# Optimization experiments

Measured on AMD Instinct MI355X. Metric: run time of the kernel, lower is better.

## Reference

```python
import jax, jax.numpy as jnp
import numpy as np

FOCUS_RADIUS = 20.0
FOCUS_WEIGHT = 10.0
SPREAD_PENALTY = 1.0
EPS = 1e-8


def setup_inputs() -> dict:
    key = jax.random.key(0)
    k1, k2 = jax.random.split(key)
    B, WL, H, W = 16, 8, 512, 512
    predictions = jax.random.uniform(k1, (B, WL, H, W), dtype=jnp.float32)
    targets = jax.random.uniform(k2, (B, WL, H, W), dtype=jnp.float32)
    return {"predictions": predictions, "targets": targets}


def reference(predictions, targets):
    B, WL, H, W = predictions.shape
    dt = predictions.dtype
    ys = jnp.arange(H, dtype=dt)[:, None]   # [H,1]
    xs = jnp.arange(W, dtype=dt)[None, :]   # [1,W]

    # base MSE loss
    base_loss = jnp.mean((predictions - targets) ** 2)

    # target energy centroids (detached in the original via .item())
    tsum = targets.sum((-2, -1))                      # [B,WL]
    valid = tsum >= EPS                               # center exists
    ts_safe = jnp.where(valid, tsum, 1.0)
    cy = jax.lax.stop_gradient((targets * ys).sum((-2, -1)) / ts_safe)  # [B,WL]
    cx = jax.lax.stop_gradient((targets * xs).sum((-2, -1)) / ts_safe)  # [B,WL]

    # squared distance to target center, per image  [B,WL,H,W]
    dist_sq = (ys - cy[..., None, None]) ** 2 + (xs - cx[..., None, None]) ** 2
    focus_mask = (dist_sq <= FOCUS_RADIUS * FOCUS_RADIUS).astype(dt)

    pred_total = predictions.sum((-2, -1))            # [B,WL]
    focus_energy = (predictions * focus_mask).sum((-2, -1))
    spread = (predictions * dist_sq).sum((-2, -1))
    pt_safe = jnp.where(pred_total > EPS, pred_total, 1.0)

    active = valid & (pred_total > EPS)
    focus_loss = jnp.sum(jnp.where(active, (1.0 - focus_energy / pt_safe) ** 2, 0.0))
    spread_loss = jnp.sum(jnp.where(active, spread / pt_safe, 0.0))

    return base_loss + FOCUS_WEIGHT * focus_loss + SPREAD_PENALTY * spread_loss
```

## Files before the change

kernel.cpp:

```cpp
#include <hip/hip_runtime.h>


#define HH 512
#define WW 512
#define IMG_PIX (HH * WW)
#define VEC_PER_IMG (IMG_PIX / 4)
#define BLOCKS_PER_IMG 16
#define VEC_PER_BLK (VEC_PER_IMG / BLOCKS_PER_IMG)
#define THREADS 256
#define ITERS (VEC_PER_BLK / THREADS)
#define EPSF 1e-8f
#define R2 400.0f

typedef float f4 __attribute__((ext_vector_type(4)));

__device__ __forceinline__ float wave_reduce_sum(float v) {
    v += __shfl_down(v, 32);
    v += __shfl_down(v, 16);
    v += __shfl_down(v, 8);
    v += __shfl_down(v, 4);
    v += __shfl_down(v, 2);
    v += __shfl_down(v, 1);
    return v;
}

__device__ __forceinline__ double wave_reduce_sum_d(double v) {
    v += __shfl_down(v, 32);
    v += __shfl_down(v, 16);
    v += __shfl_down(v, 8);
    v += __shfl_down(v, 4);
    v += __shfl_down(v, 2);
    v += __shfl_down(v, 1);
    return v;
}

__global__ void __launch_bounds__(THREADS) stream_kernel(
        const f4* __restrict__ pred, const f4* __restrict__ tgt,
        float* __restrict__ part) {
    const int img = blockIdx.x / BLOCKS_PER_IMG;
    const int sub = blockIdx.x % BLOCKS_PER_IMG;
    const int base = img * VEC_PER_IMG + sub * VEC_PER_BLK;

    float ts = 0.f, ty = 0.f, tx = 0.f, mse = 0.f;
    float m0 = 0.f, my = 0.f, mx = 0.f, m2 = 0.f;

#pragma unroll 8
    for (int j = 0; j < ITERS; ++j) {
        const int i = j * THREADS + threadIdx.x;
        const int vidx = base + i;
        const f4 tv = __builtin_nontemporal_load(&tgt[vidx]);
        const f4 pv = pred[vidx];
        const int pix = (sub * VEC_PER_BLK + i) << 2;
        const float y  = (float)(pix >> 9);
        const float x0 = (float)(pix & 511);
        const float x1 = x0 + 1.f, x2 = x0 + 2.f, x3 = x0 + 3.f;

        const float tsum = tv[0] + tv[1] + tv[2] + tv[3];
        ts += tsum;
        ty += y * tsum;
        tx += x0 * tv[0] + x1 * tv[1] + x2 * tv[2] + x3 * tv[3];

        const float d0 = pv[0] - tv[0], d1 = pv[1] - tv[1],
                    d2 = pv[2] - tv[2], d3 = pv[3] - tv[3];
        mse += d0 * d0 + d1 * d1 + d2 * d2 + d3 * d3;

        const float psum = pv[0] + pv[1] + pv[2] + pv[3];
        m0 += psum;
        my += y * psum;
        mx += x0 * pv[0] + x1 * pv[1] + x2 * pv[2] + x3 * pv[3];
        const float y2 = y * y;
        m2 += pv[0] * (y2 + x0 * x0) + pv[1] * (y2 + x1 * x1)
            + pv[2] * (y2 + x2 * x2) + pv[3] * (y2 + x3 * x3);
    }

    float vals[8] = {ts, ty, tx, mse, m0, my, mx, m2};
    __shared__ float red[4][8];
    const int wid = threadIdx.x >> 6, lane = threadIdx.x & 63;
#pragma unroll
    for (int k = 0; k < 8; ++k) vals[k] = wave_reduce_sum(vals[k]);
    if (lane == 0)
#pragma unroll
        for (int k = 0; k < 8; ++k) red[wid][k] = vals[k];
    __syncthreads();
    if (threadIdx.x < 8) {
        const int k = threadIdx.x;
        part[blockIdx.x * 8 + k] = red[0][k] + red[1][k] + red[2][k] + red[3][k];
    }
}

__global__ void __launch_bounds__(64) focus_kernel(
        const float* __restrict__ pred, const float* __restrict__ part,
        float* __restrict__ fe_out) {
    const int img = blockIdx.x;
    const int lane = threadIdx.x;
    float ts = 0.f, ty = 0.f, tx = 0.f;
    if (lane < BLOCKS_PER_IMG) {
        const float* p = part + (img * BLOCKS_PER_IMG + lane) * 8;
        ts = p[0]; ty = p[1]; tx = p[2];
    }
    ts = __shfl(wave_reduce_sum(ts), 0);
    ty = __shfl(wave_reduce_sum(ty), 0);
    tx = __shfl(wave_reduce_sum(tx), 0);

    float fe = 0.f;
    if (ts >= EPSF) {
        const float cy = ty / ts;
        const float cx = tx / ts;
        const int ylo = max(0, (int)ceilf(cy - 20.f) - 1);
        const int yhi = min(HH - 1, (int)floorf(cy + 20.f) + 1);
        const int xlo = max(0, (int)ceilf(cx - 20.f) - 1);
        const int xhi = min(WW - 1, (int)floorf(cx + 20.f) + 1);
        const float* p = pred + (size_t)img * IMG_PIX;
        const int xx = xlo + lane;
        if (xx <= xhi) {
            const float dx = (float)xx - cx;
            const float dx2 = dx * dx;
            for (int y = ylo; y <= yhi; ++y) {
                const float dy = (float)y - cy;
                if (dy * dy + dx2 <= R2) fe += p[(y << 9) + xx];
            }
        }
    }
    fe = wave_reduce_sum(fe);
    if (lane == 0) fe_out[img] = fe;
}

__global__ void __launch_bounds__(128) final_kernel(
        const float* __restrict__ part, const float* __restrict__ fe,
        float* __restrict__ out, int nimg, float inv_n) {
    const int i = threadIdx.x;
    double v = 0.0, m = 0.0;
    if (i < nimg) {
        float ts = 0.f, mse = 0.f, m0 = 0.f, myv = 0.f, mxv = 0.f, m2 = 0.f;
        float tyv = 0.f, txv = 0.f;
        const float* p = part + i * BLOCKS_PER_IMG * 8;
#pragma unroll
        for (int s = 0; s < BLOCKS_PER_IMG; ++s) {
            ts  += p[s * 8 + 0];
            tyv += p[s * 8 + 1];
            txv += p[s * 8 + 2];
            mse += p[s * 8 + 3];
            m0  += p[s * 8 + 4];
            myv += p[s * 8 + 5];
            mxv += p[s * 8 + 6];
            m2  += p[s * 8 + 7];
        }
        m = (double)mse;
        if (ts >= EPSF && m0 > EPSF) {
            const double cy = (double)tyv / (double)ts;
            const double cx = (double)txv / (double)ts;
            const double spread = (double)m2 - 2.0 * cy * (double)myv
                                - 2.0 * cx * (double)mxv
                                + (cy * cy + cx * cx) * (double)m0;
            const double r = 1.0 - (double)fe[i] / (double)m0;
            v = 10.0 * r * r + spread / (double)m0;
        }
    }
    __shared__ double redv[2], redm[2];
    v = wave_reduce_sum_d(v);
    m = wave_reduce_sum_d(m);
    if ((i & 63) == 0) { redv[i >> 6] = v; redm[i >> 6] = m; }
    __syncthreads();
    if (i == 0)
        out[0] = (float)((redm[0] + redm[1]) * (double)inv_n + redv[0] + redv[1]);
}

extern "C" void kernel_launch(void* const* d_in, const int* in_sizes, int n_in,
                              void* d_out, int out_size, void* d_ws, size_t ws_size,
                              hipStream_t stream) {
    const float* pred = (const float*)d_in[0];
    const float* tgt  = (const float*)d_in[1];
    float* out = (float*)d_out;
    float* ws  = (float*)d_ws;

    const int n = in_sizes[0];
    const int nimg = n / IMG_PIX;
    const int nblk = nimg * BLOCKS_PER_IMG;

    float* part = ws;
    float* fe   = ws + nblk * 8;

    stream_kernel<<<nblk, THREADS, 0, stream>>>(
        (const f4*)pred, (const f4*)tgt, part);
    focus_kernel<<<nimg, 64, 0, stream>>>(pred, part, fe);
    final_kernel<<<1, 128, 0, stream>>>(part, fe, out, nimg, 1.0f / (float)n);
}
```

Baseline: 63.92 us.

## Double-buffer stream loads, simplify moment math, move per-image finalization into focus kernel

The streaming kernel now prefetches the next batch of four vector loads per thread into a register double buffer while computing on the current batch. The number of blocks per image drops from 16 to 8, and the per-pixel moment arithmetic is rewritten in factored form to cut FLOPs. The focus kernel now uses 256 threads, with the four waves splitting the rows, and it computes each image's loss term, which leaves the final kernel as a simple reduction. The risks are higher register pressure from the double buffer and fewer blocks in flight to hide memory latency.

```diff
diff --git a/kernel.cpp b/kernel.cpp
--- a/kernel.cpp
+++ b/kernel.cpp
@@ -5,10 +5,12 @@
 #define WW 512
 #define IMG_PIX (HH * WW)
 #define VEC_PER_IMG (IMG_PIX / 4)
-#define BLOCKS_PER_IMG 16
+#define BLOCKS_PER_IMG 8
 #define VEC_PER_BLK (VEC_PER_IMG / BLOCKS_PER_IMG)
 #define THREADS 256
 #define ITERS (VEC_PER_BLK / THREADS)
+#define BATCH 4
+#define NBATCH (ITERS / BATCH)
 #define EPSF 1e-8f
 #define R2 400.0f
 
@@ -39,38 +41,57 @@
         float* __restrict__ part) {
     const int img = blockIdx.x / BLOCKS_PER_IMG;
     const int sub = blockIdx.x % BLOCKS_PER_IMG;
-    const int base = img * VEC_PER_IMG + sub * VEC_PER_BLK;
+    const int base = img * VEC_PER_IMG + sub * VEC_PER_BLK + (int)threadIdx.x;
+
+    f4 tb[2][BATCH], pb[2][BATCH];
+#pragma unroll
+    for (int u = 0; u < BATCH; ++u) {
+        tb[0][u] = __builtin_nontemporal_load(&tgt[base + u * THREADS]);
+        pb[0][u] = pred[base + u * THREADS];
+    }
 
     float ts = 0.f, ty = 0.f, tx = 0.f, mse = 0.f;
     float m0 = 0.f, my = 0.f, mx = 0.f, m2 = 0.f;
 
-#pragma unroll 8
-    for (int j = 0; j < ITERS; ++j) {
-        const int i = j * THREADS + threadIdx.x;
-        const int vidx = base + i;
-        const f4 tv = __builtin_nontemporal_load(&tgt[vidx]);
-        const f4 pv = pred[vidx];
-        const int pix = (sub * VEC_PER_BLK + i) << 2;
-        const float y  = (float)(pix >> 9);
-        const float x0 = (float)(pix & 511);
-        const float x1 = x0 + 1.f, x2 = x0 + 2.f, x3 = x0 + 3.f;
-
-        const float tsum = tv[0] + tv[1] + tv[2] + tv[3];
-        ts += tsum;
-        ty += y * tsum;
-        tx += x0 * tv[0] + x1 * tv[1] + x2 * tv[2] + x3 * tv[3];
-
-        const float d0 = pv[0] - tv[0], d1 = pv[1] - tv[1],
-                    d2 = pv[2] - tv[2], d3 = pv[3] - tv[3];
-        mse += d0 * d0 + d1 * d1 + d2 * d2 + d3 * d3;
-
-        const float psum = pv[0] + pv[1] + pv[2] + pv[3];
-        m0 += psum;
-        my += y * psum;
-        mx += x0 * pv[0] + x1 * pv[1] + x2 * pv[2] + x3 * pv[3];
-        const float y2 = y * y;
-        m2 += pv[0] * (y2 + x0 * x0) + pv[1] * (y2 + x1 * x1)
-            + pv[2] * (y2 + x2 * x2) + pv[3] * (y2 + x3 * x3);
+#pragma unroll
+    for (int b = 0; b < NBATCH; ++b) {
+        const int cur = b & 1, nxt = cur ^ 1;
+        if (b + 1 < NBATCH) {
+#pragma unroll
+            for (int u = 0; u < BATCH; ++u) {
+                const int v = base + ((b + 1) * BATCH + u) * THREADS;
+                tb[nxt][u] = __builtin_nontemporal_load(&tgt[v]);
+                pb[nxt][u] = pred[v];
+            }
+        }
+#pragma unroll
+        for (int u = 0; u < BATCH; ++u) {
+            const int iv = sub * VEC_PER_BLK + (b * BATCH + u) * THREADS
+                         + (int)threadIdx.x;
+            const float y  = (float)(iv >> 7);
+            const float x0 = (float)((iv & 127) << 2);
+            const f4 tv = tb[cur][u];
+            const f4 pv = pb[cur][u];
+
+            const float tsum = tv[0] + tv[1] + tv[2] + tv[3];
+            const float tw1  = tv[1] + 2.f * tv[2] + 3.f * tv[3];
+            ts += tsum;
+            ty += y * tsum;
+            tx += x0 * tsum + tw1;
+
+            const float d0 = pv[0] - tv[0], d1 = pv[1] - tv[1],
+                        d2 = pv[2] - tv[2], d3 = pv[3] - tv[3];
+            mse += d0 * d0 + d1 * d1 + d2 * d2 + d3 * d3;
+
+            const float psum = pv[0] + pv[1] + pv[2] + pv[3];
+            const float pw1  = pv[1] + 2.f * pv[2] + 3.f * pv[3];
+            const float pw2  = pv[1] + 4.f * pv[2] + 9.f * pv[3];
+            m0 += psum;
+            my += y * psum;
+            mx += x0 * psum + pw1;
+            const float r2c = y * y + x0 * x0;
+            m2 += r2c * psum + 2.f * x0 * pw1 + pw2;
+        }
     }
 
     float vals[8] = {ts, ty, tx, mse, m0, my, mx, m2};
@@ -88,81 +109,86 @@
     }
 }
 
-__global__ void __launch_bounds__(64) focus_kernel(
+__global__ void __launch_bounds__(THREADS) focus_kernel(
         const float* __restrict__ pred, const float* __restrict__ part,
-        float* __restrict__ fe_out) {
+        double* __restrict__ vout, double* __restrict__ mout) {
     const int img = blockIdx.x;
-    const int lane = threadIdx.x;
-    float ts = 0.f, ty = 0.f, tx = 0.f;
-    if (lane < BLOCKS_PER_IMG) {
-        const float* p = part + (img * BLOCKS_PER_IMG + lane) * 8;
-        ts = p[0]; ty = p[1]; tx = p[2];
-    }
-    ts = __shfl(wave_reduce_sum(ts), 0);
-    ty = __shfl(wave_reduce_sum(ty), 0);
-    tx = __shfl(wave_reduce_sum(tx), 0);
-
+    const int tid = threadIdx.x;
+    __shared__ float mom[8];
+    {
+        float v[8] = {0.f, 0.f, 0.f, 0.f, 0.f, 0.f, 0.f, 0.f};
+        if (tid < BLOCKS_PER_IMG) {
+            const float* p = part + (img * BLOCKS_PER_IMG + tid) * 8;
+#pragma unroll
+            for (int k = 0; k < 8; ++k) v[k] = p[k];
+        }
+        if (tid < 64) {
+#pragma unroll
+            for (int k = 0; k < 8; ++k) v[k] = wave_reduce_sum(v[k]);
+            if (tid == 0)
+#pragma unroll
+                for (int k = 0; k < 8; ++k) mom[k] = v[k];
+        }
+    }
+    __syncthreads();
+
+    const float ts = mom[0];
     float fe = 0.f;
+    float cy = 0.f, cx = 0.f;
     if (ts >= EPSF) {
-        const float cy = ty / ts;
-        const float cx = tx / ts;
+        cy = mom[1] / ts;
+        cx = mom[2] / ts;
         const int ylo = max(0, (int)ceilf(cy - 20.f) - 1);
         const int yhi = min(HH - 1, (int)floorf(cy + 20.f) + 1);
         const int xlo = max(0, (int)ceilf(cx - 20.f) - 1);
         const int xhi = min(WW - 1, (int)floorf(cx + 20.f) + 1);
         const float* p = pred + (size_t)img * IMG_PIX;
+        const int lane = tid & 63, w = tid >> 6;
         const int xx = xlo + lane;
         if (xx <= xhi) {
             const float dx = (float)xx - cx;
             const float dx2 = dx * dx;
-            for (int y = ylo; y <= yhi; ++y) {
+            for (int y = ylo + w; y <= yhi; y += 4) {
                 const float dy = (float)y - cy;
                 if (dy * dy + dx2 <= R2) fe += p[(y << 9) + xx];
             }
         }
     }
+    __shared__ float redf[4];
     fe = wave_reduce_sum(fe);
-    if (lane == 0) fe_out[img] = fe;
+    if ((tid & 63) == 0) redf[tid >> 6] = fe;
+    __syncthreads();
+    if (tid == 0) {
+        const float fet = redf[0] + redf[1] + redf[2] + redf[3];
+        const float m0 = mom[4];
+        double v = 0.0;
+        if (ts >= EPSF && m0 > EPSF) {
+            const double dcy = (double)mom[1] / (double)ts;
+            const double dcx = (double)mom[2] / (double)ts;
+            const double spread = (double)mom[7] - 2.0 * dcy * (double)mom[5]
+                                - 2.0 * dcx * (double)mom[6]
+                                + (dcy * dcy + dcx * dcx) * (double)m0;
+            const double r = 1.0 - (double)fet / (double)m0;
+            v = 10.0 * r * r + spread / (double)m0;
+        }
+        vout[img] = v;
+        mout[img] = (double)mom[3];
+    }
 }
 
 __global__ void __launch_bounds__(128) final_kernel(
-        const float* __restrict__ part, const float* __restrict__ fe,
-        float* __restrict__ out, int nimg, float inv_n) {
+        const double* __restrict__ vout, const double* __restrict__ mout,
+        float* __restrict__ out, int nimg, double inv_n) {
     const int i = threadIdx.x;
     double v = 0.0, m = 0.0;
-    if (i < nimg) {
-        float ts = 0.f, mse = 0.f, m0 = 0.f, myv = 0.f, mxv = 0.f, m2 = 0.f;
-        float tyv = 0.f, txv = 0.f;
-        const float* p = part + i * BLOCKS_PER_IMG * 8;
-#pragma unroll
-        for (int s = 0; s < BLOCKS_PER_IMG; ++s) {
-            ts  += p[s * 8 + 0];
-            tyv += p[s * 8 + 1];
-            txv += p[s * 8 + 2];
-            mse += p[s * 8 + 3];
-            m0  += p[s * 8 + 4];
-            myv += p[s * 8 + 5];
-            mxv += p[s * 8 + 6];
-            m2  += p[s * 8 + 7];
-        }
-        m = (double)mse;
-        if (ts >= EPSF && m0 > EPSF) {
-            const double cy = (double)tyv / (double)ts;
-            const double cx = (double)txv / (double)ts;
-            const double spread = (double)m2 - 2.0 * cy * (double)myv
-                                - 2.0 * cx * (double)mxv
-                                + (cy * cy + cx * cx) * (double)m0;
-            const double r = 1.0 - (double)fe[i] / (double)m0;
-            v = 10.0 * r * r + spread / (double)m0;
-        }
-    }
+    if (i < nimg) { v = vout[i]; m = mout[i]; }
     __shared__ double redv[2], redm[2];
     v = wave_reduce_sum_d(v);
     m = wave_reduce_sum_d(m);
     if ((i & 63) == 0) { redv[i >> 6] = v; redm[i >> 6] = m; }
     __syncthreads();
     if (i == 0)
-        out[0] = (float)((redm[0] + redm[1]) * (double)inv_n + redv[0] + redv[1]);
+        out[0] = (float)((redm[0] + redm[1]) * inv_n + redv[0] + redv[1]);
 }
 
 extern "C" void kernel_launch(void* const* d_in, const int* in_sizes, int n_in,
@@ -171,17 +197,18 @@
     const float* pred = (const float*)d_in[0];
     const float* tgt  = (const float*)d_in[1];
     float* out = (float*)d_out;
-    float* ws  = (float*)d_ws;
 
     const int n = in_sizes[0];
     const int nimg = n / IMG_PIX;
     const int nblk = nimg * BLOCKS_PER_IMG;
 
-    float* part = ws;
-    float* fe   = ws + nblk * 8;
+    float* part = (float*)d_ws;
+    double* vout = (double*)((char*)d_ws + 32768);
+    double* mout = vout + nimg;
 
     stream_kernel<<<nblk, THREADS, 0, stream>>>(
         (const f4*)pred, (const f4*)tgt, part);
-    focus_kernel<<<nimg, 64, 0, stream>>>(pred, part, fe);
-    final_kernel<<<1, 128, 0, stream>>>(part, fe, out, nimg, 1.0f / (float)n);
-}
+    focus_kernel<<<nimg, THREADS, 0, stream>>>(pred, part, vout, mout);
+    final_kernel<<<1, 128, 0, stream>>>(vout, mout, out, nimg,
+                                        1.0 / (double)n);
+}
```

Measured after the change: 65.10 us. No clear change (+1.8%).
